# Optimization experiments

Measured on AMD Instinct MI355X. Metric: run time of the kernel, lower is better.

The kernel has to match this reference:

```python
import jax, jax.numpy as jnp
import numpy as np

B = 32; NPG = 500; N = B * NPG; E = 256000; F = 1024; OD = 128
DD = 80; TD = 32; NH = 4; DH = TD // NH; DFF = 128; NL = 2
LSUB = 128; MAXLEN = 4 * LSUB
NEG = -1e9; SLOPE = 0.01; EPS = 1e-5


def setup_inputs() -> dict:
    key = jax.random.key(0)
    ks = iter(jax.random.split(key, 64))
    nrm = lambda *s: jax.random.normal(next(ks), s, jnp.float32)
    w = lambda *s: nrm(*s) * 0.02
    inp = {}
    inp["pro1_x"] = nrm(N, F)
    inp["pro2_x"] = nrm(N, F)
    inp["pro1_edge_index"] = jax.random.randint(next(ks), (2, E), 0, N)
    inp["pro2_edge_index"] = jax.random.randint(next(ks), (2, E), 0, N)
    inp["pro1_batch"] = jnp.repeat(jnp.arange(B), NPG)
    inp["pro2_batch"] = jnp.repeat(jnp.arange(B), NPG)
    for nm in ("mas1_straight", "mas1_flipped", "mas2_straight", "mas2_flipped"):
        inp[nm] = nrm(B, LSUB, DD)
        inp[nm + "_lengths"] = jax.random.randint(next(ks), (B,), 1, LSUB + 1)
    inp["gcn1_w"] = w(F, F); inp["gcn1_b"] = jnp.zeros(F)
    inp["gcn2_w"] = w(F, F); inp["gcn2_b"] = jnp.zeros(F)
    inp["fc1_w"] = w(OD, F); inp["fc1_b"] = jnp.zeros(OD)
    inp["fc2_w"] = w(OD, F); inp["fc2_b"] = jnp.zeros(OD)
    inp["red_w"] = w(TD - 2, DD); inp["red_b"] = jnp.zeros(TD - 2)
    inp["attn_in_w"] = w(NL, 3 * TD, TD); inp["attn_in_b"] = jnp.zeros((NL, 3 * TD))
    inp["attn_out_w"] = w(NL, TD, TD); inp["attn_out_b"] = jnp.zeros((NL, TD))
    inp["ln1_w"] = jnp.ones((NL, TD)); inp["ln1_b"] = jnp.zeros((NL, TD))
    inp["ln2_w"] = jnp.ones((NL, TD)); inp["ln2_b"] = jnp.zeros((NL, TD))
    inp["ff1_w"] = w(NL, DFF, TD); inp["ff1_b"] = jnp.zeros((NL, DFF))
    inp["ff2_w"] = w(NL, TD, DFF); inp["ff2_b"] = jnp.zeros((NL, TD))
    inp["final_w"] = w(1, 2 * OD + TD); inp["final_b"] = jnp.zeros(1)
    return inp


def _leaky(v):
    return jnp.where(v >= 0, v, SLOPE * v)


def _gcn(x, ei, W, b):
    # GCNConv: x' = D^-1/2 (A + I) D^-1/2 (x @ W^T) + b
    sl = jnp.arange(N, dtype=ei.dtype)
    src = jnp.concatenate([ei[0], sl])
    dst = jnp.concatenate([ei[1], sl])
    deg = jax.ops.segment_sum(jnp.ones(src.shape[0], x.dtype), dst, N)
    dinv = jax.lax.rsqrt(deg)
    norm = (dinv[src] * dinv[dst])[:, None]
    h = x @ W.T
    return jax.ops.segment_sum(h[src] * norm, dst, N) + b


def _gmp(x, batch):
    # global mean pool per graph
    s = jax.ops.segment_sum(x, batch, B)
    c = jax.ops.segment_sum(jnp.ones(x.shape[0], x.dtype), batch, B)
    return s / c[:, None]


def _ln(x, w, b):
    m = x.mean(-1, keepdims=True)
    v = ((x - m) ** 2).mean(-1, keepdims=True)
    return (x - m) * jax.lax.rsqrt(v + EPS) * w + b


def _forward(pro1_x, pro1_edge_index, pro1_batch, pro2_x, pro2_edge_index, pro2_batch,
             mas1_straight, mas1_flipped, mas2_straight, mas2_flipped,
             mas1_straight_lengths, mas1_flipped_lengths, mas2_straight_lengths, mas2_flipped_lengths,
             gcn1_w, gcn1_b, fc1_w, fc1_b, gcn2_w, gcn2_b, fc2_w, fc2_b,
             red_w, red_b, attn_in_w, attn_in_b, attn_out_w, attn_out_b,
             ln1_w, ln1_b, ln2_w, ln2_b, ff1_w, ff1_b, ff2_w, ff2_b,
             final_w, final_b):
    # --- graph branches (dropout = identity at inference) ---
    x1 = _leaky(_gcn(pro1_x, pro1_edge_index, gcn1_w, gcn1_b))
    x1 = _leaky(_gmp(x1, pro1_batch) @ fc1_w.T + fc1_b)           # [B, OD]
    x2 = _leaky(_gcn(pro2_x, pro2_edge_index, gcn2_w, gcn2_b))
    x2 = _leaky(_gmp(x2, pro2_batch) @ fc2_w.T + fc2_b)           # [B, OD]

    # --- vectorized ragged pack: project, append indicators, scatter to offsets ---
    inds = ((1.0, 1.0), (0.0, 1.0), (1.0, 0.0), (0.0, 0.0))      # (straight, first)
    mas = (mas1_straight, mas1_flipped, mas2_straight, mas2_flipped)
    lens = (mas1_straight_lengths, mas1_flipped_lengths, mas2_straight_lengths, mas2_flipped_lengths)
    pos = jnp.arange(LSUB)
    brow = jnp.arange(B)[:, None]
    seq = jnp.zeros((B, MAXLEN, TD), jnp.float32)
    off = jnp.zeros((B,), lens[0].dtype)
    for m, l, (si, fi) in zip(mas, lens, inds):
        proj = m @ red_w.T + red_b                                # [B, LSUB, TD-2]
        ones = jnp.ones((B, LSUB, 1), jnp.float32)
        p = jnp.concatenate([proj, si * ones, fi * ones], -1)    # [B, LSUB, TD]
        valid = pos[None, :] < l[:, None]                        # [B, LSUB]
        idx = jnp.where(valid, off[:, None] + pos[None, :], 0)
        seq = seq.at[brow, idx].add(p * valid[..., None])
        off = off + l
    mask = jnp.arange(MAXLEN)[None, :] < off[:, None]            # [B, MAXLEN] True = valid

    # --- post-norm TransformerEncoder (relu FFN, key padding mask) ---
    x_t = seq
    for li in range(NL):
        qkv = x_t @ attn_in_w[li].T + attn_in_b[li]
        q, k, v = jnp.split(qkv, 3, axis=-1)
        q = q.reshape(B, MAXLEN, NH, DH)
        k = k.reshape(B, MAXLEN, NH, DH)
        v = v.reshape(B, MAXLEN, NH, DH)
        scores = jnp.einsum('bqhd,bkhd->bhqk', q, k) / np.float32(np.sqrt(DH))
        scores = jnp.where(mask[:, None, None, :], scores, NEG)
        attn = jax.nn.softmax(scores, axis=-1)
        o = jnp.einsum('bhqk,bkhd->bqhd', attn, v).reshape(B, MAXLEN, TD)
        o = o @ attn_out_w[li].T + attn_out_b[li]
        x_t = _ln(x_t + o, ln1_w[li], ln1_b[li])
        h = jax.nn.relu(x_t @ ff1_w[li].T + ff1_b[li]) @ ff2_w[li].T + ff2_b[li]
        x_t = _ln(x_t + h, ln2_w[li], ln2_b[li])

    mf = mask[..., None].astype(jnp.float32)
    mas_out = (x_t * mf).sum(1) / mf.sum(1)                      # masked mean [B, TD]

    combined = jnp.concatenate([x1, x2, mas_out], axis=1)        # [B, 2*OD + TD]
    return combined @ final_w.T + final_b                        # [B, 1]


def reference(pro1_x, pro1_edge_index, pro1_batch, pro2_x, pro2_edge_index, pro2_batch,
              mas1_straight, mas1_flipped, mas2_straight, mas2_flipped,
              mas1_straight_lengths, mas1_flipped_lengths, mas2_straight_lengths, mas2_flipped_lengths,
              gcn1_w, gcn1_b, fc1_w, fc1_b, gcn2_w, gcn2_b, fc2_w, fc2_b,
              red_w, red_b, attn_in_w, attn_in_b, attn_out_w, attn_out_b,
              ln1_w, ln1_b, ln2_w, ln2_b, ff1_w, ff1_b, ff2_w, ff2_b,
              final_w, final_b):
    return _forward(pro1_x, pro1_edge_index, pro1_batch, pro2_x, pro2_edge_index, pro2_batch,
                    mas1_straight, mas1_flipped, mas2_straight, mas2_flipped,
                    mas1_straight_lengths, mas1_flipped_lengths, mas2_straight_lengths, mas2_flipped_lengths,
                    gcn1_w, gcn1_b, fc1_w, fc1_b, gcn2_w, gcn2_b, fc2_w, fc2_b,
                    red_w, red_b, attn_in_w, attn_in_b, attn_out_w, attn_out_b,
                    ln1_w, ln1_b, ln2_w, ln2_b, ff1_w, ff1_b, ff2_w, ff2_b,
                    final_w, final_b)
```

## Files before the change

### kernel.cpp

```cpp
#include <hip/hip_runtime.h>
#include <stdint.h>

#define N_NODES 16000
#define B_      32
#define NPG_    500
#define E_      256000
#define F_      1024
#define OD_     128
#define DD_     80
#define TD_     32
#define NH_     4
#define DH_     8
#define DFF_    128
#define LSUB_   128
#define MAXLEN_ 512
#define EPS_    1e-5f
#define SLOPE_  0.01f

typedef __bf16 bf16x8 __attribute__((ext_vector_type(8)));
typedef float  f32x4  __attribute__((ext_vector_type(4)));

__device__ __forceinline__ float leaky(float v) { return v >= 0.f ? v : SLOPE_ * v; }

__device__ __forceinline__ unsigned short f2bf(float f) {
  unsigned u = __float_as_uint(f);
  u += 0x7FFFu + ((u >> 16) & 1u);
  return (unsigned short)(u >> 16);
}
__device__ __forceinline__ float bf2f(unsigned short u) {
  return __uint_as_float((unsigned)u << 16);
}

__device__ __forceinline__ void gld_lds16(const void* g, void* l) {
  __builtin_amdgcn_global_load_lds(
      (const __attribute__((address_space(1))) unsigned int*)g,
      (__attribute__((address_space(3))) unsigned int*)l, 16, 0, 0);
}

__global__ void k_f2bf2(const float* __restrict__ in0, const float* __restrict__ in1,
                        unsigned short* __restrict__ out0, unsigned short* __restrict__ out1,
                        int n4) {
  const float* in = blockIdx.y ? in1 : in0;
  unsigned short* out = blockIdx.y ? out1 : out0;
  int i = blockIdx.x * blockDim.x + threadIdx.x;
  int stride = gridDim.x * blockDim.x;
  for (; i < n4; i += stride) {
    float4 v = ((const float4*)in)[i];
    ushort4 o;
    o.x = f2bf(v.x); o.y = f2bf(v.y); o.z = f2bf(v.z); o.w = f2bf(v.w);
    ((ushort4*)out)[i] = o;
  }
}

__global__ __launch_bounds__(256) void k_gemm_bf16(const unsigned short* __restrict__ A,
                                                   const unsigned short* __restrict__ Bw,
                                                   unsigned short* __restrict__ C) {
  const int K = 1024, N = 1024;
  const int id = blockIdx.x;
  const int g  = id >> 10;
  const int l  = id & 1023;
  const int xcd = l & 7;
  const int j   = l >> 3;
  const int mIdx = xcd + 8 * (j >> 3);
  const int nIdx = j & 7;
  if (mIdx >= 125) return;
  A  += (size_t)g * N_NODES * K;
  Bw += (size_t)g * K * N;
  C  += (size_t)g * N_NODES * N;
  const int mBase = mIdx * 128;
  const int nBase = nIdx * 128;

  __shared__ short As[8 * 512];
  __shared__ short Bs[8 * 512];
  const int t    = threadIdx.x;
  const int lane = t & 63, wave = t >> 6;
  const int wrow = wave >> 1, wcol = wave & 1;
  const int quad = lane >> 4, l15 = lane & 15;
  const int rI = lane & 15;
  const int cI = lane >> 4;

  f32x4 acc[4][4];
  f32x4 zero = {0.f, 0.f, 0.f, 0.f};
#pragma unroll
  for (int i = 0; i < 4; ++i)
#pragma unroll
    for (int jj = 0; jj < 4; ++jj) acc[i][jj] = zero;

  for (int kt = 0; kt < 32; ++kt) {
    const int k0 = kt * 32;
#pragma unroll
    for (int jj = 0; jj < 2; ++jj) {
      const int tile = wave * 2 + jj;
      gld_lds16(&A[(size_t)(mBase + tile * 16 + rI) * K + k0 + cI * 8],
                &As[tile * 512 + lane * 8]);
      gld_lds16(&Bw[(size_t)(nBase + tile * 16 + rI) * K + k0 + cI * 8],
                &Bs[tile * 512 + lane * 8]);
    }
    __syncthreads();

    bf16x8 a[4], b[4];
#pragma unroll
    for (int ti = 0; ti < 4; ++ti)
      a[ti] = *(const bf16x8*)&As[(wrow * 4 + ti) * 512 + quad * 128 + l15 * 8];
#pragma unroll
    for (int tj = 0; tj < 4; ++tj)
      b[tj] = *(const bf16x8*)&Bs[(wcol * 4 + tj) * 512 + quad * 128 + l15 * 8];
#pragma unroll
    for (int ti = 0; ti < 4; ++ti)
#pragma unroll
      for (int tj = 0; tj < 4; ++tj)
        acc[ti][tj] = __builtin_amdgcn_mfma_f32_16x16x32_bf16(a[ti], b[tj], acc[ti][tj], 0, 0, 0);
    __syncthreads();
  }

#pragma unroll
  for (int ti = 0; ti < 4; ++ti)
#pragma unroll
    for (int tj = 0; tj < 4; ++tj)
#pragma unroll
      for (int r = 0; r < 4; ++r) {
        int grow = mBase + wrow * 64 + ti * 16 + quad * 4 + r;
        int gcol = nBase + wcol * 64 + tj * 16 + l15;
        C[(size_t)grow * N + gcol] = f2bf(acc[ti][tj][r]);
      }
}

__global__ void k_hist(const int* __restrict__ ei0, const int* __restrict__ ei1,
                       int* __restrict__ cnt, int e, int n) {
  const int g = blockIdx.y;
  const int* dst = (g ? ei1 : ei0) + e;
  int i = blockIdx.x * 256 + threadIdx.x;
  if (i < e) atomicAdd(&cnt[g * n + dst[i]], 1);
}

__global__ void k_scan(const int* __restrict__ cnt_all, int* __restrict__ rowstart_all,
                       int* __restrict__ cursor_all, float* __restrict__ dinv_all, int n) {
  const int g = blockIdx.x;
  const int* cnt = cnt_all + g * n;
  int* rowstart = rowstart_all + g * (n + 1);
  int* cursor   = cursor_all + g * n;
  float* dinv   = dinv_all + g * n;
  __shared__ int part[256];
  __shared__ int base[257];
  int t = threadIdx.x;
  int chunk = (n + 255) >> 8;
  int s = 0;
  for (int j = 0; j < chunk; ++j) {
    int idx = t * chunk + j;
    if (idx < n) s += cnt[idx];
  }
  part[t] = s;
  __syncthreads();
  if (t == 0) {
    int a = 0;
    for (int i = 0; i < 256; ++i) { base[i] = a; a += part[i]; }
    base[256] = a;
  }
  __syncthreads();
  int a = base[t];
  for (int j = 0; j < chunk; ++j) {
    int idx = t * chunk + j;
    if (idx < n) {
      int c = cnt[idx];
      rowstart[idx] = a; cursor[idx] = a; a += c;
      dinv[idx] = rsqrtf((float)c + 1.0f);
    }
  }
  if (t == 0) rowstart[n] = base[256];
}

__global__ void k_scatter(const int* __restrict__ ei0, const int* __restrict__ ei1,
                          const float* __restrict__ dinv_all, int* __restrict__ cursor_all,
                          int* __restrict__ csr_all, float* __restrict__ csrw_all,
                          int e, int n) {
  const int g = blockIdx.y;
  const int* ei = g ? ei1 : ei0;
  int i = blockIdx.x * 256 + threadIdx.x;
  if (i < e) {
    int s = ei[i], d = ei[e + i];
    int p = atomicAdd(&cursor_all[g * n + d], 1);
    csr_all[(size_t)g * e + p]  = s;
    csrw_all[(size_t)g * e + p] = dinv_all[g * n + s] * dinv_all[g * n + d];
  }
}

__global__ __launch_bounds__(64) void k_gather(const ushort2* __restrict__ h2,
                                               const float* __restrict__ dinv,
                                               const int* __restrict__ rowstart,
                                               const int* __restrict__ csr,
                                               const float* __restrict__ csrw,
                                               ushort2* __restrict__ agg2) {
  const int sl = blockIdx.x;
  const int i  = blockIdx.y;
  const int t  = threadIdx.x;
  __shared__ int   ssrc[64];
  __shared__ float sw[64];
  const float di = dinv[i];
  const size_t fo = (size_t)sl * 64 + t;
  ushort2 sv = h2[(size_t)i * 512 + fo];
  const float selfw = di * di;
  float ax = bf2f(sv.x) * selfw, ay = bf2f(sv.y) * selfw;
  const int beg = rowstart[i], end = rowstart[i + 1];
  for (int base = beg; base < end; base += 64) {
    int c = end - base; if (c > 64) c = 64;
    __syncthreads();
    if (t < c) { ssrc[t] = csr[base + t]; sw[t] = csrw[base + t]; }
    __syncthreads();
    int j = 0;
    for (; j + 4 <= c; j += 4) {
      ushort2 v0 = h2[(size_t)ssrc[j]     * 512 + fo];
      ushort2 v1 = h2[(size_t)ssrc[j + 1] * 512 + fo];
      ushort2 v2 = h2[(size_t)ssrc[j + 2] * 512 + fo];
      ushort2 v3 = h2[(size_t)ssrc[j + 3] * 512 + fo];
      float w0 = sw[j], w1 = sw[j + 1], w2 = sw[j + 2], w3 = sw[j + 3];
      ax += bf2f(v0.x) * w0 + bf2f(v1.x) * w1 + bf2f(v2.x) * w2 + bf2f(v3.x) * w3;
      ay += bf2f(v0.y) * w0 + bf2f(v1.y) * w1 + bf2f(v2.y) * w2 + bf2f(v3.y) * w3;
    }
    for (; j < c; ++j) {
      ushort2 v0 = h2[(size_t)ssrc[j] * 512 + fo];
      float w0 = sw[j];
      ax += bf2f(v0.x) * w0; ay += bf2f(v0.y) * w0;
    }
  }
  ushort2 o; o.x = f2bf(ax); o.y = f2bf(ay);
  agg2[(size_t)i * 512 + fo] = o;
}

__global__ void k_pool(const unsigned short* __restrict__ agg_all,
                       const float* __restrict__ bias0, const float* __restrict__ bias1,
                       float* __restrict__ pooled_all) {
  int f = blockIdx.x * 256 + threadIdx.x;
  int z = blockIdx.z;
  int g = z >> 5, b = z & 31;
  const unsigned short* agg = agg_all + (size_t)g * N_NODES * F_;
  const float* bias = g ? bias1 : bias0;
  float* pooled = pooled_all + (size_t)g * B_ * F_;
  int r0 = blockIdx.y * 100;
  float bf = bias[f];
  float s = 0.f;
  for (int r = 0; r < 100; ++r)
    s += leaky(bf2f(agg[(size_t)(b * NPG_ + r0 + r) * F_ + f]) + bf);
  atomicAdd(&pooled[b * F_ + f], s);
}

__global__ void k_fc(const float* __restrict__ pooled_all,
                     const float* __restrict__ w0, const float* __restrict__ w1,
                     const float* __restrict__ bias0, const float* __restrict__ bias1,
                     float* __restrict__ out0, float* __restrict__ out1) {
  int b = blockIdx.x, o = threadIdx.x, g = blockIdx.y;
  const float* p  = pooled_all + (size_t)g * B_ * F_ + b * F_;
  const float* wr = (g ? w1 : w0) + o * F_;
  const float* bias = g ? bias1 : bias0;
  float* out = g ? out1 : out0;
  float acc = 0.f;
  for (int f = 0; f < F_; ++f) acc += p[f] * wr[f];
  out[b * OD_ + o] = leaky(acc * (1.f / 500.f) + bias[o]);
}

__global__ void k_pack(const float* __restrict__ m0, const float* __restrict__ m1,
                       const float* __restrict__ m2, const float* __restrict__ m3,
                       const int* __restrict__ l0, const int* __restrict__ l1,
                       const int* __restrict__ l2, const int* __restrict__ l3,
                       const float* __restrict__ rw, const float* __restrict__ rb,
                       float* __restrict__ seq) {
  __shared__ float xs[DD_];
  const int p = blockIdx.x, b = blockIdx.y, k = blockIdx.z;
  const float* mas = (k == 0) ? m0 : (k == 1) ? m1 : (k == 2) ? m2 : m3;
  const int*   lk  = (k == 0) ? l0 : (k == 1) ? l1 : (k == 2) ? l2 : l3;
  const int len = lk[b];
  if (p >= len) return;
  int off = 0;
  if (k > 0) off += l0[b];
  if (k > 1) off += l1[b];
  if (k > 2) off += l2[b];
  const int t = threadIdx.x;
  for (int d = t; d < DD_; d += 64) xs[d] = mas[(size_t)(b * LSUB_ + p) * DD_ + d];
  __syncthreads();
  if (t < TD_) {
    float v;
    if (t < TD_ - 2) {
      float a = rb[t];
      const float* w = &rw[t * DD_];
      for (int d = 0; d < DD_; ++d) a += xs[d] * w[d];
      v = a;
    } else if (t == TD_ - 2) {
      v = (k == 0 || k == 2) ? 1.f : 0.f;
    } else {
      v = (k < 2) ? 1.f : 0.f;
    }
    seq[((size_t)b * MAXLEN_ + off + p) * TD_ + t] = v;
  }
}

__global__ void k_totlen(const int* __restrict__ l0, const int* __restrict__ l1,
                         const int* __restrict__ l2, const int* __restrict__ l3,
                         int* __restrict__ tot) {
  int b = threadIdx.x;
  if (b < B_) tot[b] = l0[b] + l1[b] + l2[b] + l3[b];
}

__global__ void k_qkv(const float* __restrict__ xt, const float* __restrict__ w,
                      const float* __restrict__ bias, const int* __restrict__ tot,
                      float* __restrict__ qkv) {
  __shared__ float xs[TD_];
  const int row = blockIdx.x;
  if ((row & (MAXLEN_ - 1)) >= tot[row >> 9]) return;
  const int t = threadIdx.x;
  if (t < TD_) xs[t] = xt[(size_t)row * TD_ + t];
  __syncthreads();
  if (t < 3 * TD_) {
    float a = bias[t];
    const float* wr = &w[t * TD_];
#pragma unroll
    for (int k = 0; k < TD_; ++k) a += xs[k] * wr[k];
    qkv[(size_t)row * 96 + t] = a;
  }
}

__global__ __launch_bounds__(128) void k_attn(const float* __restrict__ qkv,
                                              const int* __restrict__ tot,
                                              float* __restrict__ obuf) {
  __shared__ float Kl[MAXLEN_ * DH_];
  __shared__ float Vl[MAXLEN_ * DH_];
  const int h = blockIdx.x, b = blockIdx.y, qz = blockIdx.z;
  const int t = threadIdx.x;
  const int L = tot[b];
  if (qz * 64 >= L) return;
  const float* base = &qkv[(size_t)b * MAXLEN_ * 96];
  for (int i = t; i < L * DH_; i += 128) {
    int p = i >> 3, d = i & 7;
    Kl[i] = base[p * 96 + 32 + h * 8 + d];
    Vl[i] = base[p * 96 + 64 + h * 8 + d];
  }
  __syncthreads();
  const int qi = qz * 64 + (t >> 1);
  if (qi >= L) return;
  const int half = t & 1;
  const float scale = 0.35355339059327373f;
  float q[8];
#pragma unroll
  for (int d = 0; d < 8; ++d) q[d] = base[qi * 96 + h * 8 + d] * scale;

  float l0 = 0.f, l1 = 0.f;
  float a0[8] = {0, 0, 0, 0, 0, 0, 0, 0};
  float a1[8] = {0, 0, 0, 0, 0, 0, 0, 0};
  int j = half;
  for (; j + 2 < L; j += 4) {
    const float* kr0 = &Kl[j * 8];
    const float* kr1 = &Kl[(j + 2) * 8];
    float s0 = 0.f, s1 = 0.f;
#pragma unroll
    for (int d = 0; d < 8; ++d) { s0 += q[d] * kr0[d]; s1 += q[d] * kr1[d]; }
    float p0 = __expf(s0), p1 = __expf(s1);
    l0 += p0; l1 += p1;
    const float* vr0 = &Vl[j * 8];
    const float* vr1 = &Vl[(j + 2) * 8];
#pragma unroll
    for (int d = 0; d < 8; ++d) { a0[d] += p0 * vr0[d]; a1[d] += p1 * vr1[d]; }
  }
  for (; j < L; j += 2) {
    const float* kr = &Kl[j * 8];
    float s = 0.f;
#pragma unroll
    for (int d = 0; d < 8; ++d) s += q[d] * kr[d];
    float p = __expf(s);
    l0 += p;
    const float* vr = &Vl[j * 8];
#pragma unroll
    for (int d = 0; d < 8; ++d) a0[d] += p * vr[d];
  }
  float l = l0 + l1;
#pragma unroll
  for (int d = 0; d < 8; ++d) a0[d] += a1[d];
  l += __shfl_xor(l, 1);
#pragma unroll
  for (int d = 0; d < 8; ++d) a0[d] += __shfl_xor(a0[d], 1);
  float inv = 1.f / l;
  const int dbase = half * 4;
  float4 o;
  o.x = a0[dbase + 0] * inv; o.y = a0[dbase + 1] * inv;
  o.z = a0[dbase + 2] * inv; o.w = a0[dbase + 3] * inv;
  *(float4*)&obuf[((size_t)b * MAXLEN_ + qi) * TD_ + h * 8 + dbase] = o;
}

__global__ void k_oproj_ln(const float* __restrict__ obuf, const float* __restrict__ w,
                           const float* __restrict__ bias, const float* __restrict__ lw,
                           const float* __restrict__ lb, const int* __restrict__ tot,
                           float* __restrict__ xt) {
  const int t = threadIdx.x;
  const int r = blockIdx.x * 8 + (t >> 5);
  if ((r & (MAXLEN_ - 1)) >= tot[r >> 9]) return;
  const int j = t & 31;
  const float* orow = &obuf[(size_t)r * TD_];
  float a = bias[j] + xt[(size_t)r * TD_ + j];
  const float* wr = &w[j * TD_];
#pragma unroll
  for (int k = 0; k < TD_; ++k) a += orow[k] * wr[k];
  float s1 = a, s2 = a * a;
#pragma unroll
  for (int m = 1; m < 32; m <<= 1) {
    s1 += __shfl_xor(s1, m, 32);
    s2 += __shfl_xor(s2, m, 32);
  }
  float mean = s1 * (1.f / 32.f);
  float var  = s2 * (1.f / 32.f) - mean * mean;
  xt[(size_t)r * TD_ + j] = (a - mean) * rsqrtf(var + EPS_) * lw[j] + lb[j];
}

__global__ void k_ffn_ln(const float* __restrict__ w1, const float* __restrict__ b1,
                         const float* __restrict__ w2, const float* __restrict__ b2,
                         const float* __restrict__ lw, const float* __restrict__ lb,
                         const int* __restrict__ tot, float* __restrict__ xt) {
  const int r = blockIdx.x, t = threadIdx.x;
  if ((r & (MAXLEN_ - 1)) >= tot[r >> 9]) return;
  __shared__ float xs[TD_];
  __shared__ float hb[DFF_];
  if (t < TD_) xs[t] = xt[(size_t)r * TD_ + t];
  __syncthreads();
  {
    float a = b1[t];
    const float* wr = &w1[t * TD_];
#pragma unroll
    for (int k = 0; k < TD_; ++k) a += xs[k] * wr[k];
    hb[t] = fmaxf(a, 0.f);
  }
  __syncthreads();
  if (t < TD_) {
    float a = b2[t] + xs[t];
    const float* wr = &w2[t * DFF_];
#pragma unroll
    for (int k = 0; k < DFF_; ++k) a += hb[k] * wr[k];
    float s1 = a, s2 = a * a;
#pragma unroll
    for (int m = 1; m < 32; m <<= 1) {
      s1 += __shfl_xor(s1, m, 32);
      s2 += __shfl_xor(s2, m, 32);
    }
    float mean = s1 * (1.f / 32.f);
    float var  = s2 * (1.f / 32.f) - mean * mean;
    xt[(size_t)r * TD_ + t] = (a - mean) * rsqrtf(var + EPS_) * lw[t] + lb[t];
  }
}

__global__ void k_maskmean(const float* __restrict__ xt, const int* __restrict__ tot,
                           float* __restrict__ mout) {
  __shared__ float sbuf[8][32];
  const int b = blockIdx.x, t = threadIdx.x;
  const int j = t & 31, c = t >> 5;
  const int L = tot[b];
  float s = 0.f;
  for (int p = c; p < L; p += 8) s += xt[((size_t)b * MAXLEN_ + p) * TD_ + j];
  sbuf[c][j] = s;
  __syncthreads();
  if (t < 32) {
    float a = 0.f;
#pragma unroll
    for (int cc = 0; cc < 8; ++cc) a += sbuf[cc][t];
    mout[b * TD_ + t] = a / (float)L;
  }
}

__global__ void k_final(const float* __restrict__ x1, const float* __restrict__ x2,
                        const float* __restrict__ mo, const float* __restrict__ fw,
                        const float* __restrict__ fb, float* __restrict__ out) {
  const int b = blockIdx.x, t = threadIdx.x;
  float s = 0.f;
  for (int i = t; i < 2 * OD_ + TD_; i += 64) {
    float c = (i < OD_) ? x1[b * OD_ + i]
            : (i < 2 * OD_) ? x2[b * OD_ + (i - OD_)]
            : mo[b * TD_ + (i - 2 * OD_)];
    s += fw[i] * c;
  }
#pragma unroll
  for (int m = 1; m < 64; m <<= 1) s += __shfl_xor(s, m, 64);
  if (t == 0) out[b] = s + fb[0];
}

extern "C" void kernel_launch(void* const* d_in, const int* in_sizes, int n_in,
                              void* d_out, int out_size, void* d_ws, size_t ws_size,
                              hipStream_t stream) {
  (void)in_sizes; (void)n_in; (void)out_size; (void)ws_size;
  const float* pro_x[2]  = {(const float*)d_in[0], (const float*)d_in[1]};
  const int*   pro_ei[2] = {(const int*)d_in[2], (const int*)d_in[3]};
  const float* mas[4]    = {(const float*)d_in[6], (const float*)d_in[8],
                            (const float*)d_in[10], (const float*)d_in[12]};
  const int*   lens[4]   = {(const int*)d_in[7], (const int*)d_in[9],
                            (const int*)d_in[11], (const int*)d_in[13]};
  const float* gw[2]  = {(const float*)d_in[14], (const float*)d_in[16]};
  const float* gb[2]  = {(const float*)d_in[15], (const float*)d_in[17]};
  const float* fcw[2] = {(const float*)d_in[18], (const float*)d_in[20]};
  const float* fcb[2] = {(const float*)d_in[19], (const float*)d_in[21]};
  const float* red_w = (const float*)d_in[22];
  const float* red_b = (const float*)d_in[23];
  const float* attn_in_w  = (const float*)d_in[24];
  const float* attn_in_b  = (const float*)d_in[25];
  const float* attn_out_w = (const float*)d_in[26];
  const float* attn_out_b = (const float*)d_in[27];
  const float* ln1_w = (const float*)d_in[28];
  const float* ln1_b = (const float*)d_in[29];
  const float* ln2_w = (const float*)d_in[30];
  const float* ln2_b = (const float*)d_in[31];
  const float* ff1_w = (const float*)d_in[32];
  const float* ff1_b = (const float*)d_in[33];
  const float* ff2_w = (const float*)d_in[34];
  const float* ff2_b = (const float*)d_in[35];
  const float* final_w = (const float*)d_in[36];
  const float* final_b = (const float*)d_in[37];
  float* out = (float*)d_out;

  char* p = (char*)d_ws;
  auto carve = [&](size_t bytes) -> void* {
    void* r = (void*)p;
    p += (bytes + 255) & ~(size_t)255;
    return r;
  };
  unsigned short* xb  = (unsigned short*)carve((size_t)2 * N_NODES * F_ * 2);
  unsigned short* Wb  = (unsigned short*)carve((size_t)2 * F_ * F_ * 2);
  unsigned short* h   = (unsigned short*)carve((size_t)2 * N_NODES * F_ * 2);
  unsigned short* agg = (unsigned short*)carve((size_t)2 * N_NODES * F_ * 2);
  int*   cnt      = (int*)carve((size_t)2 * N_NODES * 4);
  float* dinv     = (float*)carve((size_t)2 * N_NODES * 4);
  int*   rowstart = (int*)carve((size_t)2 * (N_NODES + 1) * 4);
  int*   cursor   = (int*)carve((size_t)2 * N_NODES * 4);
  int*   csr      = (int*)carve((size_t)2 * E_ * 4);
  float* csrw     = (float*)carve((size_t)2 * E_ * 4);
  float* pooled   = (float*)carve((size_t)2 * B_ * F_ * 4);
  float* xg[2];
  xg[0] = (float*)carve((size_t)B_ * OD_ * 4);
  xg[1] = (float*)carve((size_t)B_ * OD_ * 4);
  float* seq    = (float*)carve((size_t)B_ * MAXLEN_ * TD_ * 4);
  float* qkv    = (float*)carve((size_t)B_ * MAXLEN_ * 96 * 4);
  float* obuf   = (float*)carve((size_t)B_ * MAXLEN_ * TD_ * 4);
  int*   totlen = (int*)carve((size_t)B_ * 4);
  float* masout = (float*)carve((size_t)B_ * TD_ * 4);

  k_f2bf2<<<dim3(1024, 2), 256, 0, stream>>>(pro_x[0], pro_x[1], xb,
                                             xb + (size_t)N_NODES * F_, (N_NODES * F_) / 4);
  k_f2bf2<<<dim3(512, 2), 256, 0, stream>>>(gw[0], gw[1], Wb, Wb + (size_t)F_ * F_,
                                            (F_ * F_) / 4);
  k_gemm_bf16<<<2048, 256, 0, stream>>>(xb, Wb, h);
  hipMemsetAsync(cnt, 0, (size_t)2 * N_NODES * 4, stream);
  k_hist<<<dim3(1000, 2), 256, 0, stream>>>(pro_ei[0], pro_ei[1], cnt, E_, N_NODES);
  k_scan<<<2, 256, 0, stream>>>(cnt, rowstart, cursor, dinv, N_NODES);
  k_scatter<<<dim3(1000, 2), 256, 0, stream>>>(pro_ei[0], pro_ei[1], dinv, cursor,
                                               csr, csrw, E_, N_NODES);
  for (int g = 0; g < 2; ++g) {
    k_gather<<<dim3(8, N_NODES), 64, 0, stream>>>(
        (const ushort2*)(h + (size_t)g * N_NODES * F_), dinv + (size_t)g * N_NODES,
        rowstart + (size_t)g * (N_NODES + 1), csr + (size_t)g * E_, csrw + (size_t)g * E_,
        (ushort2*)(agg + (size_t)g * N_NODES * F_));
  }
  hipMemsetAsync(pooled, 0, (size_t)2 * B_ * F_ * 4, stream);
  k_pool<<<dim3(4, 5, 64), 256, 0, stream>>>(agg, gb[0], gb[1], pooled);
  k_fc<<<dim3(B_, 2), 128, 0, stream>>>(pooled, fcw[0], fcw[1], fcb[0], fcb[1],
                                        xg[0], xg[1]);

  hipMemsetAsync(seq, 0, (size_t)B_ * MAXLEN_ * TD_ * 4, stream);
  k_pack<<<dim3(LSUB_, B_, 4), 64, 0, stream>>>(mas[0], mas[1], mas[2], mas[3],
                                                lens[0], lens[1], lens[2], lens[3],
                                                red_w, red_b, seq);
  k_totlen<<<1, 64, 0, stream>>>(lens[0], lens[1], lens[2], lens[3], totlen);

  for (int li = 0; li < 2; ++li) {
    k_qkv<<<B_ * MAXLEN_, 128, 0, stream>>>(seq, attn_in_w + (size_t)li * 96 * TD_,
                                            attn_in_b + (size_t)li * 96, totlen, qkv);
    k_attn<<<dim3(NH_, B_, 8), 128, 0, stream>>>(qkv, totlen, obuf);
    k_oproj_ln<<<(B_ * MAXLEN_) / 8, 256, 0, stream>>>(
        obuf, attn_out_w + (size_t)li * TD_ * TD_, attn_out_b + (size_t)li * TD_,
        ln1_w + (size_t)li * TD_, ln1_b + (size_t)li * TD_, totlen, seq);
    k_ffn_ln<<<B_ * MAXLEN_, 128, 0, stream>>>(
        ff1_w + (size_t)li * DFF_ * TD_, ff1_b + (size_t)li * DFF_,
        ff2_w + (size_t)li * TD_ * DFF_, ff2_b + (size_t)li * TD_,
        ln2_w + (size_t)li * TD_, ln2_b + (size_t)li * TD_, totlen, seq);
  }

  k_maskmean<<<B_, 256, 0, stream>>>(seq, totlen, masout);
  k_final<<<B_, 64, 0, stream>>>(xg[0], xg[1], masout, final_w, final_b, out);
}
```

Baseline: 844.6 us.

## Double-buffer LDS tiles in bf16 GEMM to overlap global loads with MFMA

The GCN feature GEMM now uses two LDS buffers for the A and B tiles. The next K-slice is prefetched with global-to-LDS loads right after the barrier, while MFMAs run on the current buffer. This cuts the loop to one barrier per iteration and hides global load latency behind compute. In exchange, shared memory per block doubles, which may lower occupancy.

```diff
diff --git a/kernel.cpp b/kernel.cpp
--- a/kernel.cpp
+++ b/kernel.cpp
@@ -70,8 +70,8 @@
   const int mBase = mIdx * 128;
   const int nBase = nIdx * 128;
 
-  __shared__ short As[8 * 512];
-  __shared__ short Bs[8 * 512];
+  __shared__ short As[2][8 * 512];
+  __shared__ short Bs[2][8 * 512];
   const int t    = threadIdx.x;
   const int lane = t & 63, wave = t >> 6;
   const int wrow = wave >> 1, wcol = wave & 1;
@@ -86,31 +86,41 @@
 #pragma unroll
     for (int jj = 0; jj < 4; ++jj) acc[i][jj] = zero;
 
+  const int tile0 = wave * 2, tile1 = wave * 2 + 1;
+  const unsigned short* aP0 = &A[(size_t)(mBase + tile0 * 16 + rI) * K + cI * 8];
+  const unsigned short* aP1 = &A[(size_t)(mBase + tile1 * 16 + rI) * K + cI * 8];
+  const unsigned short* bP0 = &Bw[(size_t)(nBase + tile0 * 16 + rI) * K + cI * 8];
+  const unsigned short* bP1 = &Bw[(size_t)(nBase + tile1 * 16 + rI) * K + cI * 8];
+
+  gld_lds16(aP0, &As[0][tile0 * 512 + lane * 8]);
+  gld_lds16(aP1, &As[0][tile1 * 512 + lane * 8]);
+  gld_lds16(bP0, &Bs[0][tile0 * 512 + lane * 8]);
+  gld_lds16(bP1, &Bs[0][tile1 * 512 + lane * 8]);
+
   for (int kt = 0; kt < 32; ++kt) {
-    const int k0 = kt * 32;
-#pragma unroll
-    for (int jj = 0; jj < 2; ++jj) {
-      const int tile = wave * 2 + jj;
-      gld_lds16(&A[(size_t)(mBase + tile * 16 + rI) * K + k0 + cI * 8],
-                &As[tile * 512 + lane * 8]);
-      gld_lds16(&Bw[(size_t)(nBase + tile * 16 + rI) * K + k0 + cI * 8],
-                &Bs[tile * 512 + lane * 8]);
+    const int cur = kt & 1;
+    __syncthreads();
+    if (kt + 1 < 32) {
+      const int nxt = cur ^ 1;
+      const int k1 = (kt + 1) * 32;
+      gld_lds16(aP0 + k1, &As[nxt][tile0 * 512 + lane * 8]);
+      gld_lds16(aP1 + k1, &As[nxt][tile1 * 512 + lane * 8]);
+      gld_lds16(bP0 + k1, &Bs[nxt][tile0 * 512 + lane * 8]);
+      gld_lds16(bP1 + k1, &Bs[nxt][tile1 * 512 + lane * 8]);
     }
-    __syncthreads();
 
     bf16x8 a[4], b[4];
 #pragma unroll
     for (int ti = 0; ti < 4; ++ti)
-      a[ti] = *(const bf16x8*)&As[(wrow * 4 + ti) * 512 + quad * 128 + l15 * 8];
+      a[ti] = *(const bf16x8*)&As[cur][(wrow * 4 + ti) * 512 + quad * 128 + l15 * 8];
 #pragma unroll
     for (int tj = 0; tj < 4; ++tj)
-      b[tj] = *(const bf16x8*)&Bs[(wcol * 4 + tj) * 512 + quad * 128 + l15 * 8];
+      b[tj] = *(const bf16x8*)&Bs[cur][(wcol * 4 + tj) * 512 + quad * 128 + l15 * 8];
 #pragma unroll
     for (int ti = 0; ti < 4; ++ti)
 #pragma unroll
       for (int tj = 0; tj < 4; ++tj)
         acc[ti][tj] = __builtin_amdgcn_mfma_f32_16x16x32_bf16(a[ti], b[tj], acc[ti][tj], 0, 0, 0);
-    __syncthreads();
   }
 
 #pragma unroll
```

Result: no change. 849.2 us (+0.5%).

## Load GEMM fragments directly from global into registers with double buffering

Applied to the files above, without the earlier changes.

The bf16 GEMM no longer stages A and B tiles through LDS with global_load_lds and two barriers per k-step. Each wave now loads its own MFMA operand fragments straight from global memory into registers, prefetching the next k-slice while the current one feeds the MFMAs, and the k-loop is fully unrolled. This removes LDS traffic and block-wide synchronisation. In exchange, operand reuse across waves now depends on L1/L2 rather than shared memory, so global load volume rises (each A/B fragment is loaded by two waves), and register pressure grows.

```diff
diff --git a/kernel.cpp b/kernel.cpp
--- a/kernel.cpp
+++ b/kernel.cpp
@@ -31,12 +31,6 @@
   return __uint_as_float((unsigned)u << 16);
 }
 
-__device__ __forceinline__ void gld_lds16(const void* g, void* l) {
-  __builtin_amdgcn_global_load_lds(
-      (const __attribute__((address_space(1))) unsigned int*)g,
-      (__attribute__((address_space(3))) unsigned int*)l, 16, 0, 0);
-}
-
 __global__ void k_f2bf2(const float* __restrict__ in0, const float* __restrict__ in1,
                         unsigned short* __restrict__ out0, unsigned short* __restrict__ out1,
                         int n4) {
@@ -67,17 +61,20 @@
   A  += (size_t)g * N_NODES * K;
   Bw += (size_t)g * K * N;
   C  += (size_t)g * N_NODES * N;
-  const int mBase = mIdx * 128;
-  const int nBase = nIdx * 128;
-
-  __shared__ short As[8 * 512];
-  __shared__ short Bs[8 * 512];
   const int t    = threadIdx.x;
   const int lane = t & 63, wave = t >> 6;
   const int wrow = wave >> 1, wcol = wave & 1;
   const int quad = lane >> 4, l15 = lane & 15;
-  const int rI = lane & 15;
-  const int cI = lane >> 4;
+  const int mBase = mIdx * 128;
+  const int nBase = nIdx * 128;
+
+  const unsigned short* aP[4];
+  const unsigned short* bP[4];
+#pragma unroll
+  for (int i = 0; i < 4; ++i) {
+    aP[i] = &A[(size_t)(mBase + wrow * 64 + i * 16 + l15) * K + quad * 8];
+    bP[i] = &Bw[(size_t)(nBase + wcol * 64 + i * 16 + l15) * K + quad * 8];
+  }
 
   f32x4 acc[4][4];
   f32x4 zero = {0.f, 0.f, 0.f, 0.f};
@@ -86,31 +83,30 @@
 #pragma unroll
     for (int jj = 0; jj < 4; ++jj) acc[i][jj] = zero;
 
+  bf16x8 aR[2][4], bR[2][4];
+#pragma unroll
+  for (int i = 0; i < 4; ++i) {
+    aR[0][i] = *(const bf16x8*)aP[i];
+    bR[0][i] = *(const bf16x8*)bP[i];
+  }
+
+#pragma unroll
   for (int kt = 0; kt < 32; ++kt) {
-    const int k0 = kt * 32;
-#pragma unroll
-    for (int jj = 0; jj < 2; ++jj) {
-      const int tile = wave * 2 + jj;
-      gld_lds16(&A[(size_t)(mBase + tile * 16 + rI) * K + k0 + cI * 8],
-                &As[tile * 512 + lane * 8]);
-      gld_lds16(&Bw[(size_t)(nBase + tile * 16 + rI) * K + k0 + cI * 8],
-                &Bs[tile * 512 + lane * 8]);
+    const int cur = kt & 1, nxt = cur ^ 1;
+    if (kt < 31) {
+      const int off = (kt + 1) * 32;
+#pragma unroll
+      for (int i = 0; i < 4; ++i) {
+        aR[nxt][i] = *(const bf16x8*)(aP[i] + off);
+        bR[nxt][i] = *(const bf16x8*)(bP[i] + off);
+      }
     }
-    __syncthreads();
-
-    bf16x8 a[4], b[4];
 #pragma unroll
     for (int ti = 0; ti < 4; ++ti)
-      a[ti] = *(const bf16x8*)&As[(wrow * 4 + ti) * 512 + quad * 128 + l15 * 8];
-#pragma unroll
-    for (int tj = 0; tj < 4; ++tj)
-      b[tj] = *(const bf16x8*)&Bs[(wcol * 4 + tj) * 512 + quad * 128 + l15 * 8];
-#pragma unroll
-    for (int ti = 0; ti < 4; ++ti)
 #pragma unroll
       for (int tj = 0; tj < 4; ++tj)
-        acc[ti][tj] = __builtin_amdgcn_mfma_f32_16x16x32_bf16(a[ti], b[tj], acc[ti][tj], 0, 0, 0);
-    __syncthreads();
+        acc[ti][tj] = __builtin_amdgcn_mfma_f32_16x16x32_bf16(aR[cur][ti], bR[cur][tj],
+                                                              acc[ti][tj], 0, 0, 0);
   }
 
 #pragma unroll
```

Measured after the change: 949.6 us. +12.4%, slower.
